# Kernel tuning notes

Measured on AMD Instinct MI355X. Metric: run time of the kernel, lower is better.

The kernel has to match this reference:

```python
import jax, jax.numpy as jnp
import numpy as np
import math

# ---- GPT-OSS attention config (gpt-oss-20b) ----
HIDDEN = 2880
HEAD_DIM = 64
N_Q_HEADS = 64
N_KV_HEADS = 8
GROUP = N_Q_HEADS // N_KV_HEADS  # 8
WINDOW = 128                      # sliding window (keys in (q-128, q])
ROPE_BASE = 150000.0
SCALING_FACTOR = 32.0
NTK_ALPHA = 1.0
NTK_BETA = 32.0
INIT_CTX = 4096
Q_SIZE = N_Q_HEADS * HEAD_DIM     # 4096
KV_SIZE = N_KV_HEADS * HEAD_DIM   # 512
SM_SCALE = HEAD_DIM ** -0.5


def _yarn_inv_freq_and_concentration():
    """YaRN-scaled inverse frequencies (matches GptOssRotaryEmbedding)."""
    d_half = HEAD_DIM / 2
    freq = ROPE_BASE ** (np.arange(0, HEAD_DIM, 2, dtype=np.float32) / HEAD_DIM)
    concentration = 0.1 * math.log(SCALING_FACTOR) + 1.0
    low = d_half * math.log(INIT_CTX / (NTK_BETA * 2 * math.pi)) / math.log(ROPE_BASE)
    high = d_half * math.log(INIT_CTX / (NTK_ALPHA * 2 * math.pi)) / math.log(ROPE_BASE)
    interpolation = 1.0 / (SCALING_FACTOR * freq)
    extrapolation = 1.0 / freq
    ramp = (np.arange(d_half, dtype=np.float32) - low) / (high - low)
    mask = 1.0 - np.clip(ramp, 0.0, 1.0)
    inv_freq = interpolation * (1.0 - mask) + extrapolation * mask
    return jnp.asarray(inv_freq, jnp.float32), jnp.float32(concentration)

_INV_FREQ, _CONC = _yarn_inv_freq_and_concentration()


def _apply_rope(x, cos, sin):
    # x: [n, h, d]; cos/sin: [n, d/2] (neox style: rotate halves)
    d2 = HEAD_DIM // 2
    x1, x2 = x[..., :d2], x[..., d2:]
    c, s = cos[:, None, :], sin[:, None, :]
    return jnp.concatenate([x1 * c - x2 * s, x2 * c + x1 * s], axis=-1)


def setup_inputs() -> dict:
    key = jax.random.key(0)
    ks = jax.random.split(key, 6)
    n = 8192
    return {
        "hidden_states": jax.random.normal(ks[0], (n, HIDDEN), jnp.float32),
        "position_ids": jnp.arange(n, dtype=jnp.int32),
        "qkv_w": jax.random.normal(ks[1], (Q_SIZE + 2 * KV_SIZE, HIDDEN), jnp.float32) * (HIDDEN ** -0.5),
        "qkv_b": jax.random.normal(ks[2], (Q_SIZE + 2 * KV_SIZE,), jnp.float32) * 0.02,
        "o_w": jax.random.normal(ks[3], (HIDDEN, Q_SIZE), jnp.float32) * (Q_SIZE ** -0.5),
        "o_b": jax.random.normal(ks[4], (HIDDEN,), jnp.float32) * 0.02,
        "sinks": jax.random.normal(ks[5], (N_Q_HEADS,), jnp.float32),
    }


def reference(hidden_states, position_ids, qkv_w, qkv_b, o_w, o_b, sinks):
    n = hidden_states.shape[0]
    W = WINDOW
    nb = n // W  # n must be a multiple of the window (8192 / 128 = 64)

    # QKV projection
    qkv = hidden_states @ qkv_w.T + qkv_b
    q = qkv[:, :Q_SIZE].reshape(n, N_Q_HEADS, HEAD_DIM)
    k = qkv[:, Q_SIZE:Q_SIZE + KV_SIZE].reshape(n, N_KV_HEADS, HEAD_DIM)
    v = qkv[:, Q_SIZE + KV_SIZE:].reshape(n, N_KV_HEADS, HEAD_DIM)

    # RoPE (YaRN, neox)
    angles = position_ids.astype(jnp.float32)[:, None] * _INV_FREQ[None, :]
    cos = jnp.cos(angles) * _CONC
    sin = jnp.sin(angles) * _CONC
    q = _apply_rope(q, cos, sin)
    k = _apply_rope(k, cos, sin)

    # Blocked sliding-window attention: each W-block of queries attends to
    # [previous block, own block] keys (window=W keys incl. self).
    qb = (q * SM_SCALE).reshape(nb, W, N_KV_HEADS, GROUP, HEAD_DIM)
    kb = k.reshape(nb, W, N_KV_HEADS, HEAD_DIM)
    vb = v.reshape(nb, W, N_KV_HEADS, HEAD_DIM)
    k2 = jnp.concatenate([jnp.concatenate([jnp.zeros_like(kb[:1]), kb[:-1]], 0), kb], axis=1)  # [nb,2W,Hk,d]
    v2 = jnp.concatenate([jnp.concatenate([jnp.zeros_like(vb[:1]), vb[:-1]], 0), vb], axis=1)

    # scores: [nb, Hk, G, W, 2W]
    scores = jnp.einsum('bqgjd,bkgd->bgjqk', qb, k2)

    # mask: key global idx = (b-1)*W + j; need 0 <= q-k <= W-1 and k >= 0
    i = jnp.arange(W)[:, None]
    j = jnp.arange(2 * W)[None, :]
    mrel = (j >= i + 1) & (j <= i + W)                       # [W, 2W]
    first = (jnp.arange(nb)[:, None, None] > 0) | (j >= W)   # [nb, 1|W, 2W]
    mask = (mrel[None] & first)[:, None, None, :, :]          # [nb,1,1,W,2W]

    neg_inf = jnp.float32(-jnp.inf)
    s = jnp.where(mask, scores, neg_inf)
    sink = sinks.reshape(N_KV_HEADS, GROUP)[None, :, :, None]  # [1,Hk,G,1]
    m = jnp.maximum(jnp.max(s, axis=-1), sink)                  # [nb,Hk,G,W]
    e = jnp.exp(s - m[..., None])
    denom = e.sum(axis=-1) + jnp.exp(sink - m)                  # sink adds to denominator only
    p = e / denom[..., None]

    out = jnp.einsum('bgjqk,bkgd->bqgjd', p, v2).reshape(n, Q_SIZE)
    return out @ o_w.T + o_b
```

## Files before the change

### kernel.cpp

```cpp
#include <hip/hip_runtime.h>
#include <math.h>
#include <stdint.h>

typedef float  f32x4  __attribute__((ext_vector_type(4)));
typedef __bf16 bf16x8 __attribute__((ext_vector_type(8)));
typedef __bf16 bf16x4 __attribute__((ext_vector_type(4)));
typedef unsigned int u32x4 __attribute__((ext_vector_type(4)));

#define MFMA16(a, b, c) __builtin_amdgcn_mfma_f32_16x16x32_bf16(a, b, c, 0, 0, 0)

__device__ __forceinline__ void async16(const void* g, void* l) {
  __builtin_amdgcn_global_load_lds((__attribute__((address_space(1))) void*)g,
                                   (__attribute__((address_space(3))) void*)l,
                                   16, 0, 0);
}

__device__ __forceinline__ bf16x8 dsr16(const void* p) {
  u32x4 r;
  asm volatile("ds_read_b128 %0, %1"
               : "=v"(r)
               : "v"((__attribute__((address_space(3))) const void*)p));
  union { u32x4 u; bf16x8 b; } c;
  c.u = r;
  return c.b;
}

__global__ __launch_bounds__(256) void cast_f32_to_bf16(const float* __restrict__ in,
                                                        __bf16* __restrict__ out, int n) {
  int idx = (blockIdx.x * 256 + threadIdx.x) * 4;
  if (idx + 3 < n) {
    float4 v = *(const float4*)(in + idx);
    bf16x4 o;
    o[0] = (__bf16)v.x; o[1] = (__bf16)v.y; o[2] = (__bf16)v.z; o[3] = (__bf16)v.w;
    *(bf16x4*)(out + idx) = o;
  }
}

__global__ __launch_bounds__(256) void rope_table_kernel(const int* __restrict__ pos_ids,
                                                         float2* __restrict__ tab, int total) {
  int idx = blockIdx.x * 256 + threadIdx.x;
  if (idx >= total) return;
  int p = idx >> 5, d = idx & 31;
  float posf = (float)pos_ids[p];
  float ex = (float)(2 * d) * (1.0f / 64.0f);
  float freq = powf(150000.0f, ex);
  float inv_scaled = 1.0f / (32.0f * freq);
  float inv_plain = 1.0f / freq;
  float lr = logf(150000.0f);
  const float TWO_PI = 6.28318530717958647692f;
  float low  = 32.0f * logf(4096.0f / (32.0f * TWO_PI)) / lr;
  float high = 32.0f * logf(4096.0f / TWO_PI) / lr;
  float ramp = ((float)d - low) / (high - low);
  ramp = fminf(fmaxf(ramp, 0.0f), 1.0f);
  float maskv = 1.0f - ramp;
  float inv_freq = inv_scaled * (1.0f - maskv) + inv_plain * maskv;
  float conc = 0.1f * logf(32.0f) + 1.0f;
  float ang = posf * inv_freq;
  float s, c;
  sincosf(ang, &s, &c);
  tab[idx] = make_float2(c * conc, s * conc);
}

template <typename OutT, bool DO_ROPE>
__global__ __launch_bounds__(512, 2) void gemm256(const __bf16* __restrict__ A,
                                                  const __bf16* __restrict__ B,
                                                  const float* __restrict__ bias,
                                                  OutT* __restrict__ C,
                                                  const float2* __restrict__ tab,
                                                  int M, int N, int K) {
  __shared__ __align__(16) __bf16 lds_all[65536];
  __bf16* Asl = lds_all;
  __bf16* Bsl = lds_all + 32768;

  const int tid = threadIdx.x;
  const int wv  = tid >> 6;
  const int ln  = tid & 63;
  const int l16 = ln & 15;
  const int quad = ln >> 4;
  const int wr = wv >> 2;
  const int wc = wv & 3;

  const int nTN = (N + 255) >> 8;
  int bid = (int)blockIdx.x;
  int nwg = (int)gridDim.x;
  int swz = bid;
  if ((nwg & 7) == 0) {
    int cpx = nwg >> 3;
    swz = (bid & 7) * cpx + (bid >> 3);
  }
  const int brow = swz / nTN;
  const int bcol = swz % nTN;
  const int row0 = brow << 8, col0 = bcol << 8;

  const int rsw  = (l16 >> 1) & 3;
  const int aoff = (wr * 128 + l16) * 32 + ((quad ^ rsw) * 8);
  const int boff = (wc * 64 + l16) * 32 + ((quad ^ rsw) * 8);

  const int srow = tid >> 2;
  const int skq  = (tid & 3) ^ ((tid >> 3) & 3);

  auto stA = [&](int t_, int kh) {
    const __bf16* s = A + (size_t)(row0 + srow) * K + t_ * 64 + kh * 32 + skq * 8;
    char* d = (char*)Asl + (((2 * t_ + kh) & 3) << 14) + (wv << 10);
    async16(s, d);
    async16(s + (size_t)128 * K, d + 8192);
  };
  auto stB = [&](int t_, int kh) {
    int r0 = col0 + srow;       if (r0 > N - 1) r0 = N - 1;
    int r1 = col0 + srow + 128; if (r1 > N - 1) r1 = N - 1;
    const int kb = t_ * 64 + kh * 32 + skq * 8;
    char* d = (char*)Bsl + (((2 * t_ + kh) & 3) << 14) + (wv << 10);
    async16(B + (size_t)r0 * K + kb, d);
    async16(B + (size_t)r1 * K + kb, d + 8192);
  };

  f32x4 acc[8][4];
#pragma unroll
  for (int t = 0; t < 8; t++)
#pragma unroll
    for (int u = 0; u < 4; u++) acc[t][u] = (f32x4){0.f, 0.f, 0.f, 0.f};

  const int nt = K >> 6;

  stA(0, 0); stB(0, 0); stA(0, 1); stB(0, 1);
  if (nt > 1) {
    stA(1, 0); stB(1, 0); stA(1, 1); stB(1, 1);
    asm volatile("s_waitcnt vmcnt(4)" ::: "memory");
  } else {
    asm volatile("s_waitcnt vmcnt(0)" ::: "memory");
  }
  __builtin_amdgcn_s_barrier();

#define PHASE_TAIL()                                      \
  __builtin_amdgcn_s_barrier();                           \
  asm volatile("s_waitcnt lgkmcnt(0)" ::: "memory");      \
  __builtin_amdgcn_sched_barrier(0);                      \
  __builtin_amdgcn_s_setprio(1);

#define PHASE_END()                                       \
  __builtin_amdgcn_s_setprio(0);                          \
  __builtin_amdgcn_s_barrier();

#pragma unroll 1
  for (int t = 0; t < nt; ++t) {
    const __bf16* As0 = Asl + (((2 * t) & 3) << 13);
    const __bf16* Bs0 = Bsl + (((2 * t) & 3) << 13);
    const __bf16* As1 = Asl + (((2 * t + 1) & 3) << 13);
    const __bf16* Bs1 = Bsl + (((2 * t + 1) & 3) << 13);
    bf16x8 a[4], b[4];

#pragma unroll
    for (int i = 0; i < 4; ++i) a[i] = dsr16(As0 + aoff + i * 512);
#pragma unroll
    for (int u = 0; u < 4; ++u) b[u] = dsr16(Bs0 + boff + u * 512);
    if (t >= 1 && t + 1 < nt) stA(t + 1, 1);
    PHASE_TAIL();
#pragma unroll
    for (int i = 0; i < 4; ++i)
#pragma unroll
      for (int u = 0; u < 4; ++u) acc[i][u] = MFMA16(a[i], b[u], acc[i][u]);
    PHASE_END();

#pragma unroll
    for (int i = 0; i < 4; ++i) a[i] = dsr16(As0 + aoff + (4 + i) * 512);
    if (t >= 1 && t + 1 < nt) stB(t + 1, 1);
    PHASE_TAIL();
#pragma unroll
    for (int i = 0; i < 4; ++i)
#pragma unroll
      for (int u = 0; u < 4; ++u) acc[4 + i][u] = MFMA16(a[i], b[u], acc[4 + i][u]);
    PHASE_END();

#pragma unroll
    for (int i = 0; i < 4; ++i) a[i] = dsr16(As1 + aoff + i * 512);
#pragma unroll
    for (int u = 0; u < 4; ++u) b[u] = dsr16(Bs1 + boff + u * 512);
    if (t + 2 < nt) stA(t + 2, 0);
    PHASE_TAIL();
#pragma unroll
    for (int i = 0; i < 4; ++i)
#pragma unroll
      for (int u = 0; u < 4; ++u) acc[i][u] = MFMA16(a[i], b[u], acc[i][u]);
    PHASE_END();

#pragma unroll
    for (int i = 0; i < 4; ++i) a[i] = dsr16(As1 + aoff + (4 + i) * 512);
    if (t + 2 < nt) {
      stB(t + 2, 0);
      asm volatile("s_waitcnt vmcnt(4)" ::: "memory");
    } else {
      asm volatile("s_waitcnt vmcnt(0)" ::: "memory");
    }
    PHASE_TAIL();
#pragma unroll
    for (int i = 0; i < 4; ++i)
#pragma unroll
      for (int u = 0; u < 4; ++u) acc[4 + i][u] = MFMA16(a[i], b[u], acc[4 + i][u]);
    PHASE_END();
  }
#undef PHASE_TAIL
#undef PHASE_END

  const int hh = (col0 + wc * 64) >> 6;
  if (DO_ROPE && hh < 72) {
    const float scale = hh < 64 ? 0.125f : 1.0f;
    float bv[4];
#pragma unroll
    for (int u = 0; u < 4; u++) bv[u] = bias[col0 + wc * 64 + u * 16 + l16];
#pragma unroll
    for (int tt = 0; tt < 8; ++tt) {
      int rowb = row0 + wr * 128 + tt * 16 + quad * 4;
#pragma unroll
      for (int r = 0; r < 4; r++) {
        int row = rowb + r;
#pragma unroll
        for (int u = 0; u < 2; u++) {
          float2 cs = tab[row * 32 + u * 16 + l16];
          float x1 = acc[tt][u][r] + bv[u];
          float x2 = acc[tt][u + 2][r] + bv[u + 2];
          C[(size_t)row * N + col0 + wc * 64 + u * 16 + l16] =
              (OutT)((x1 * cs.x - x2 * cs.y) * scale);
          C[(size_t)row * N + col0 + wc * 64 + (u + 2) * 16 + l16] =
              (OutT)((x2 * cs.x + x1 * cs.y) * scale);
        }
      }
    }
  } else {
#pragma unroll
    for (int u = 0; u < 4; u++) {
      int col = col0 + wc * 64 + u * 16 + l16;
      if (col < N) {
        float bv = bias[col];
#pragma unroll
        for (int tt = 0; tt < 8; ++tt) {
          int row = row0 + wr * 128 + tt * 16 + quad * 4;
#pragma unroll
          for (int r = 0; r < 4; r++)
            C[(size_t)(row + r) * N + col] = (OutT)(acc[tt][u][r] + bv);
        }
      }
    }
  }
}

__global__ __launch_bounds__(256) void attn_kernel(const __bf16* __restrict__ qkv,
                                                   const float* __restrict__ sinks,
                                                   __bf16* __restrict__ out) {
  __shared__ __align__(16) __bf16 vT_s[64 * 264];
  __shared__ __align__(16) __bf16 k_s[256 * 64];
  __shared__ __align__(16) __bf16 p_s[64 * 72];
  const int tid = threadIdx.x;
  const int bh = blockIdx.x >> 1;
  const int qh = blockIdx.x & 1;
  const int b = bh >> 3;
  const int h = bh & 7;
  const int wv = tid >> 6;
  const int ln = tid & 63;
  const int l16 = ln & 15;
  const int quad = ln >> 4;

  for (int c = tid; c < 2048; c += 256) {
    int key = c >> 3, dc = c & 7;
    int pos = b * 128 + key - 128;
    bf16x8 vv = {}, kk = {};
    if (pos >= 0) {
      const __bf16* base = qkv + (size_t)pos * 5120 + h * 64 + dc * 8;
      kk = *(const bf16x8*)(base + 4096);
      vv = *(const bf16x8*)(base + 4608);
    }
    int keysw = key ^ ((dc & 3) << 3);
#pragma unroll
    for (int l2 = 0; l2 < 8; l2++)
      vT_s[(dc * 8 + l2) * 264 + keysw] = vv[l2];
    *(bf16x8*)&k_s[key * 64 + ((dc ^ (key & 7)) * 8)] = kk;
  }
  __syncthreads();

#pragma unroll 1
  for (int pass = 0; pass < 8; pass++) {
    int g = qh * 4 + (pass >> 1);
    int i0 = (pass & 1) * 64 + wv * 16;
    int head = h * 8 + g;
    float sink = sinks[head];

    size_t qbase = (size_t)(b * 128 + i0 + l16) * 5120 + head * 64;
    bf16x8 aq0 = *(const bf16x8*)(qkv + qbase + quad * 8);
    bf16x8 aq1 = *(const bf16x8*)(qkv + qbase + 32 + quad * 8);

    f32x4 sc[16];
    const int sw0 = (quad ^ (l16 & 7)) * 8;
#pragma unroll
    for (int ct = 0; ct < 16; ct++) {
      const __bf16* kp = &k_s[(ct * 16 + l16) * 64];
      bf16x8 kb0 = *(const bf16x8*)(kp + sw0);
      bf16x8 kb1 = *(const bf16x8*)(kp + (sw0 ^ 32));
      f32x4 z = (f32x4){0.f, 0.f, 0.f, 0.f};
      __builtin_amdgcn_s_setprio(1);
      z = MFMA16(aq0, kb0, z);
      z = MFMA16(aq1, kb1, z);
      __builtin_amdgcn_s_setprio(0);
      sc[ct] = z;
    }

    float mx[4] = {-INFINITY, -INFINITY, -INFINITY, -INFINITY};
#pragma unroll
    for (int ct = 0; ct < 16; ct++) {
      int j = ct * 16 + l16;
#pragma unroll
      for (int r = 0; r < 4; r++) {
        int i = i0 + quad * 4 + r;
        bool valid = (j >= i + 1) && (j <= i + 128) && (b > 0 || j >= 128);
        float s = valid ? sc[ct][r] : -INFINITY;
        sc[ct][r] = s;
        mx[r] = fmaxf(mx[r], s);
      }
    }
#pragma unroll
    for (int off = 1; off < 16; off <<= 1)
#pragma unroll
      for (int r = 0; r < 4; r++)
        mx[r] = fmaxf(mx[r], __shfl_xor(mx[r], off));
#pragma unroll
    for (int r = 0; r < 4; r++) mx[r] = fmaxf(mx[r], sink);

    float sum[4] = {0.f, 0.f, 0.f, 0.f};
#pragma unroll
    for (int ct = 0; ct < 16; ct++)
#pragma unroll
      for (int r = 0; r < 4; r++) {
        float e = __expf(sc[ct][r] - mx[r]);
        sc[ct][r] = e;
        sum[r] += e;
      }
#pragma unroll
    for (int off = 1; off < 16; off <<= 1)
#pragma unroll
      for (int r = 0; r < 4; r++)
        sum[r] += __shfl_xor(sum[r], off);

    f32x4 o[4];
#pragma unroll
    for (int dt = 0; dt < 4; dt++) o[dt] = (f32x4){0.f, 0.f, 0.f, 0.f};
#pragma unroll
    for (int q = 0; q < 4; q++) {
#pragma unroll
      for (int ct = 0; ct < 4; ct++)
#pragma unroll
        for (int r = 0; r < 4; r++)
          p_s[(wv * 16 + quad * 4 + r) * 72 + ct * 16 + l16] = (__bf16)sc[q * 4 + ct][r];
#pragma unroll
      for (int ks = 0; ks < 2; ks++) {
        bf16x8 pa = *(const bf16x8*)&p_s[(wv * 16 + l16) * 72 + ks * 32 + quad * 8];
        __builtin_amdgcn_s_setprio(1);
#pragma unroll
        for (int dt = 0; dt < 4; dt++) {
          int kk = q * 64 + ks * 32 + quad * 8;
          int sw = ((dt * 2 + (l16 >> 3)) & 3) << 3;
          bf16x8 vb = *(const bf16x8*)&vT_s[(dt * 16 + l16) * 264 + (kk ^ sw)];
          o[dt] = MFMA16(pa, vb, o[dt]);
        }
        __builtin_amdgcn_s_setprio(0);
      }
    }

#pragma unroll
    for (int r = 0; r < 4; r++) {
      float rd = 1.0f / (sum[r] + __expf(sink - mx[r]));
      int posn = b * 128 + i0 + quad * 4 + r;
      size_t obase = (size_t)posn * 4096 + head * 64;
#pragma unroll
      for (int dt = 0; dt < 4; dt++)
        out[obase + dt * 16 + l16] = (__bf16)(o[dt][r] * rd);
    }
  }
}

extern "C" void kernel_launch(void* const* d_in, const int* in_sizes, int n_in,
                              void* d_out, int out_size, void* d_ws, size_t ws_size,
                              hipStream_t stream) {
  (void)in_sizes; (void)n_in; (void)out_size; (void)ws_size;
  const float* hs     = (const float*)d_in[0];
  const int*   pos    = (const int*)d_in[1];
  const float* qkv_w  = (const float*)d_in[2];
  const float* qkv_b  = (const float*)d_in[3];
  const float* o_w    = (const float*)d_in[4];
  const float* o_b    = (const float*)d_in[5];
  const float* sinks  = (const float*)d_in[6];
  float* outp = (float*)d_out;
  char* ws = (char*)d_ws;

  const size_t O_QKV = 0;
  const size_t O_ATT = 83886080;
  const size_t O_TAB = 131072000;
  const size_t O_W   = 150994944;
  __bf16* qkvb = (__bf16*)(ws + O_QKV);
  __bf16* hsb  = (__bf16*)(ws + O_ATT);
  __bf16* attn = (__bf16*)(ws + O_ATT);
  float2* tab  = (float2*)(ws + O_TAB);
  __bf16* wb   = (__bf16*)(ws + O_W);

  cast_f32_to_bf16<<<23040, 256, 0, stream>>>(hs, hsb, 8192 * 2880);
  cast_f32_to_bf16<<<14400, 256, 0, stream>>>(qkv_w, wb, 5120 * 2880);
  rope_table_kernel<<<1024, 256, 0, stream>>>(pos, tab, 8192 * 32);
  gemm256<__bf16, true><<<640, 512, 0, stream>>>(hsb, wb, qkv_b, qkvb, tab,
                                                 8192, 5120, 2880);
  cast_f32_to_bf16<<<11520, 256, 0, stream>>>(o_w, wb, 2880 * 4096);
  attn_kernel<<<1024, 256, 0, stream>>>(qkvb, sinks, attn);
  gemm256<float, false><<<384, 512, 0, stream>>>(attn, wb, o_b, outp, nullptr,
                                                 8192, 2880, 4096);
}
```

Measured before the change: 815.4 us.

## Double-buffer LDS fragment registers and overlap reads with MFMA phases

Restructures the GEMM main loop so LDS fragment reads for the next phase are issued before the current phase's MFMAs, using two register sets (a0/a1, bb0/bb1) and partial lgkmcnt waits instead of full drains. It also removes one barrier per phase and changes the global-load prefetch schedule (second half-tile of stage 1 loaded inside the loop). The aim is to hide LDS latency behind matrix work. The cost is extra VGPR pressure and more delicate vmcnt/lgkmcnt accounting, which could cause hazards or lower occupancy.

```diff
diff --git a/kernel.cpp b/kernel.cpp
--- a/kernel.cpp
+++ b/kernel.cpp
@@ -124,22 +124,18 @@
 
   stA(0, 0); stB(0, 0); stA(0, 1); stB(0, 1);
   if (nt > 1) {
-    stA(1, 0); stB(1, 0); stA(1, 1); stB(1, 1);
+    stA(1, 0); stB(1, 0);
     asm volatile("s_waitcnt vmcnt(4)" ::: "memory");
   } else {
     asm volatile("s_waitcnt vmcnt(0)" ::: "memory");
   }
   __builtin_amdgcn_s_barrier();
 
-#define PHASE_TAIL()                                      \
-  __builtin_amdgcn_s_barrier();                           \
-  asm volatile("s_waitcnt lgkmcnt(0)" ::: "memory");      \
-  __builtin_amdgcn_sched_barrier(0);                      \
-  __builtin_amdgcn_s_setprio(1);
-
-#define PHASE_END()                                       \
-  __builtin_amdgcn_s_setprio(0);                          \
-  __builtin_amdgcn_s_barrier();
+  bf16x8 a0[4], a1[4], bb0[4], bb1[4];
+#pragma unroll
+  for (int i = 0; i < 4; ++i) a0[i] = dsr16(Asl + aoff + i * 512);
+#pragma unroll
+  for (int u = 0; u < 4; ++u) bb0[u] = dsr16(Bsl + boff + u * 512);
 
 #pragma unroll 1
   for (int t = 0; t < nt; ++t) {
@@ -147,59 +143,75 @@
     const __bf16* Bs0 = Bsl + (((2 * t) & 3) << 13);
     const __bf16* As1 = Asl + (((2 * t + 1) & 3) << 13);
     const __bf16* Bs1 = Bsl + (((2 * t + 1) & 3) << 13);
-    bf16x8 a[4], b[4];
-
-#pragma unroll
-    for (int i = 0; i < 4; ++i) a[i] = dsr16(As0 + aoff + i * 512);
-#pragma unroll
-    for (int u = 0; u < 4; ++u) b[u] = dsr16(Bs0 + boff + u * 512);
-    if (t >= 1 && t + 1 < nt) stA(t + 1, 1);
-    PHASE_TAIL();
+    const __bf16* AsN = Asl + (((2 * t + 2) & 3) << 13);
+    const __bf16* BsN = Bsl + (((2 * t + 2) & 3) << 13);
+    const bool st1 = (t + 1 < nt);
+    const bool st2 = (t + 2 < nt);
+
+    if (st1) stA(t + 1, 1);
+#pragma unroll
+    for (int i = 0; i < 4; ++i) a1[i] = dsr16(As0 + aoff + (4 + i) * 512);
+    asm volatile("s_waitcnt lgkmcnt(4)" ::: "memory");
+    __builtin_amdgcn_sched_barrier(0);
+    __builtin_amdgcn_s_setprio(1);
 #pragma unroll
     for (int i = 0; i < 4; ++i)
 #pragma unroll
-      for (int u = 0; u < 4; ++u) acc[i][u] = MFMA16(a[i], b[u], acc[i][u]);
-    PHASE_END();
-
-#pragma unroll
-    for (int i = 0; i < 4; ++i) a[i] = dsr16(As0 + aoff + (4 + i) * 512);
-    if (t >= 1 && t + 1 < nt) stB(t + 1, 1);
-    PHASE_TAIL();
+      for (int u = 0; u < 4; ++u) acc[i][u] = MFMA16(a0[i], bb0[u], acc[i][u]);
+    __builtin_amdgcn_s_setprio(0);
+    __builtin_amdgcn_s_barrier();
+
+    if (st1) stB(t + 1, 1);
+#pragma unroll
+    for (int i = 0; i < 4; ++i) a0[i] = dsr16(As1 + aoff + i * 512);
+#pragma unroll
+    for (int u = 0; u < 4; ++u) bb1[u] = dsr16(Bs1 + boff + u * 512);
+    asm volatile("s_waitcnt lgkmcnt(8)" ::: "memory");
+    __builtin_amdgcn_sched_barrier(0);
+    __builtin_amdgcn_s_setprio(1);
 #pragma unroll
     for (int i = 0; i < 4; ++i)
 #pragma unroll
-      for (int u = 0; u < 4; ++u) acc[4 + i][u] = MFMA16(a[i], b[u], acc[4 + i][u]);
-    PHASE_END();
-
-#pragma unroll
-    for (int i = 0; i < 4; ++i) a[i] = dsr16(As1 + aoff + i * 512);
-#pragma unroll
-    for (int u = 0; u < 4; ++u) b[u] = dsr16(Bs1 + boff + u * 512);
-    if (t + 2 < nt) stA(t + 2, 0);
-    PHASE_TAIL();
+      for (int u = 0; u < 4; ++u) acc[4 + i][u] = MFMA16(a1[i], bb0[u], acc[4 + i][u]);
+    __builtin_amdgcn_s_setprio(0);
+    __builtin_amdgcn_s_barrier();
+
+    if (st2) stA(t + 2, 0);
+#pragma unroll
+    for (int i = 0; i < 4; ++i) a1[i] = dsr16(As1 + aoff + (4 + i) * 512);
+    asm volatile("s_waitcnt lgkmcnt(4)" ::: "memory");
+    __builtin_amdgcn_sched_barrier(0);
+    __builtin_amdgcn_s_setprio(1);
 #pragma unroll
     for (int i = 0; i < 4; ++i)
 #pragma unroll
-      for (int u = 0; u < 4; ++u) acc[i][u] = MFMA16(a[i], b[u], acc[i][u]);
-    PHASE_END();
-
-#pragma unroll
-    for (int i = 0; i < 4; ++i) a[i] = dsr16(As1 + aoff + (4 + i) * 512);
-    if (t + 2 < nt) {
-      stB(t + 2, 0);
-      asm volatile("s_waitcnt vmcnt(4)" ::: "memory");
+      for (int u = 0; u < 4; ++u) acc[i][u] = MFMA16(a0[i], bb1[u], acc[i][u]);
+    __builtin_amdgcn_s_setprio(0);
+    if (st2) { asm volatile("s_waitcnt vmcnt(6)" ::: "memory"); }
+    else     { asm volatile("s_waitcnt vmcnt(4)" ::: "memory"); }
+    __builtin_amdgcn_s_barrier();
+
+    if (st2) stB(t + 2, 0);
+    if (st1) {
+#pragma unroll
+      for (int i = 0; i < 4; ++i) a0[i] = dsr16(AsN + aoff + i * 512);
+#pragma unroll
+      for (int u = 0; u < 4; ++u) bb0[u] = dsr16(BsN + boff + u * 512);
+      asm volatile("s_waitcnt lgkmcnt(8)" ::: "memory");
     } else {
-      asm volatile("s_waitcnt vmcnt(0)" ::: "memory");
-    }
-    PHASE_TAIL();
+      asm volatile("s_waitcnt lgkmcnt(0)" ::: "memory");
+    }
+    __builtin_amdgcn_sched_barrier(0);
+    __builtin_amdgcn_s_setprio(1);
 #pragma unroll
     for (int i = 0; i < 4; ++i)
 #pragma unroll
-      for (int u = 0; u < 4; ++u) acc[4 + i][u] = MFMA16(a[i], b[u], acc[4 + i][u]);
-    PHASE_END();
-  }
-#undef PHASE_TAIL
-#undef PHASE_END
+      for (int u = 0; u < 4; ++u) acc[4 + i][u] = MFMA16(a1[i], bb1[u], acc[4 + i][u]);
+    __builtin_amdgcn_s_setprio(0);
+    if (st2) { asm volatile("s_waitcnt vmcnt(4)" ::: "memory"); }
+    else     { asm volatile("s_waitcnt vmcnt(0)" ::: "memory"); }
+    __builtin_amdgcn_s_barrier();
+  }
 
   const int hh = (col0 + wc * 64) >> 6;
   if (DO_ROPE && hh < 72) {
```

After: 800.2 us. About the same (-1.9%).
